# Performance work log

Hardware: AMD Instinct MI355X
Metric: run time of the kernel (lower is better)

Reference implementation:

```python
import jax, jax.numpy as jnp
import numpy as np

B, IN, OUT, STY = 8192, 2048, 2048, 512

def setup_inputs() -> dict:
    key = jax.random.key(0)
    k1, k2, k3, k4, k5 = jax.random.split(key, 5)
    bound_w = 1.0 / np.sqrt(IN)  # kaiming_uniform(a=sqrt(5)) on (OUT,IN) -> U(-1/sqrt(IN), 1/sqrt(IN))
    weight = jax.random.uniform(k1, (OUT, IN), jnp.float32, -bound_w, bound_w)
    bias = jax.random.uniform(k2, (OUT,), jnp.float32, -bound_w, bound_w)
    bound_a = 1.0 / np.sqrt(STY)
    aff_w = jax.random.uniform(k3, (2 * OUT, STY), jnp.float32, -bound_a, bound_a)
    aff_b = jnp.concatenate([jnp.ones((OUT,), jnp.float32), jnp.zeros((OUT,), jnp.float32)])
    inp = jax.random.normal(k4, (B, IN), jnp.float32)
    style = jax.random.normal(k5, (B, STY), jnp.float32)
    return {"input": inp, "style": style, "weight": weight, "bias": bias,
            "aff_w": aff_w, "aff_b": aff_b}

def reference(input, style, weight, bias, aff_w, aff_b):
    # affine: (B, 2*OUT), chunk into scale / (unused) style-bias
    enc = style @ aff_w.T + aff_b
    scale = enc[:, :OUT]  # (B, OUT); second chunk is discarded by the original forward
    # Original math: w1 = W * s[b,o]; norm = rsqrt(sum_i w1^2); w2 = w1 / norm = w1 * sqrt(sum_i w1^2)
    # sum_i (W[o,i]*s[b,o])^2 = s[b,o]^2 * rowsq[o]  ->  w2[b,o,i] = W[o,i] * s*|s| * sqrt(rowsq[o])
    rowsq = jnp.sum(weight * weight, axis=1)                  # (OUT,)
    mod = scale * jnp.abs(scale) * jnp.sqrt(rowsq)[None, :]   # (B, OUT)
    base = input @ weight.T                                   # (B, OUT) single GEMM
    return base * mod + bias[None, :]
```

## Files before the change

### kernel.cpp

```cpp
#include <hip/hip_runtime.h>
#include <cstdint>
#include <cstddef>

#define B_ROWS 8192
#define IN_DIM 2048
#define OUT_DIM 2048
#define STY_DIM 512

#define BM 128
#define BN 128
#define BK 32
#define PAD_K 40

typedef unsigned short u16;
typedef __attribute__((ext_vector_type(8))) short bf16x8;
typedef __attribute__((ext_vector_type(4))) float f32x4;

__device__ __forceinline__ void cvt_pair(float x0, float x1, uint32_t& hi, uint32_t& lo) {
  uint32_t u0 = __float_as_uint(x0), u1 = __float_as_uint(x1);
  uint32_t a0 = u0 & 0xffff0000u, a1 = u1 & 0xffff0000u;
  hi = (u0 >> 16) | a1;
  float l0 = x0 - __uint_as_float(a0);
  float l1 = x1 - __uint_as_float(a1);
  lo = (__float_as_uint(l0) >> 16) | (__float_as_uint(l1) & 0xffff0000u);
}

__device__ __forceinline__ void write_rep(const float4& v, u16* baseHi, u16* baseLo) {
  uint32_t h0, h1, l0, l1;
  cvt_pair(v.x, v.y, h0, l0);
  cvt_pair(v.z, v.w, h1, l1);
  uint2 hw; hw.x = h0; hw.y = h1;
  uint2 lw; lw.x = l0; lw.y = l1;
  *reinterpret_cast<uint2*>(baseHi) = hw;
  *reinterpret_cast<uint2*>(baseLo) = lw;
}

template<int LDK, int NT>
__device__ __forceinline__ void gemm_phase(
    const float* __restrict__ gA, const float* __restrict__ gB,
    f32x4 (&acc)[4][4],
    u16* sAhi, u16* sAlo, u16* sBhi, u16* sBlo,
    int tid)
{
  const int sr = tid >> 3;
  const int sk = (tid & 7) * 4;
  const float* pa = gA + (size_t)sr * LDK + sk;
  const float* pb = gB + (size_t)sr * LDK + sk;
  const int lbase = sr * PAD_K + sk;

  const int lane = tid & 63;
  const int wid  = tid >> 6;
  const int wr = wid >> 1, wc = wid & 1;
  const int fr = lane & 15;
  const int kg = lane >> 4;
  const int aoff = (wr * 64 + fr) * PAD_K + kg * 8;
  const int boff = (wc * 64 + fr) * PAD_K + kg * 8;

  float4 va[4], vb[4];
  #pragma unroll
  for (int rep = 0; rep < 4; ++rep) {
    va[rep] = *reinterpret_cast<const float4*>(pa + (size_t)rep * 32 * LDK);
    vb[rep] = *reinterpret_cast<const float4*>(pb + (size_t)rep * 32 * LDK);
  }
  pa += BK; pb += BK;

  for (int t = 0; t < NT; ++t) {
    __syncthreads();
    #pragma unroll
    for (int rep = 0; rep < 4; ++rep) {
      write_rep(va[rep], sAhi + lbase + rep * 32 * PAD_K, sAlo + lbase + rep * 32 * PAD_K);
      write_rep(vb[rep], sBhi + lbase + rep * 32 * PAD_K, sBlo + lbase + rep * 32 * PAD_K);
    }
    __syncthreads();
    if (t + 1 < NT) {
      #pragma unroll
      for (int rep = 0; rep < 4; ++rep) {
        va[rep] = *reinterpret_cast<const float4*>(pa + (size_t)rep * 32 * LDK);
        vb[rep] = *reinterpret_cast<const float4*>(pb + (size_t)rep * 32 * LDK);
      }
      pa += BK; pb += BK;
    }

    bf16x8 bhi[4], blo[4];
    #pragma unroll
    for (int nj = 0; nj < 4; ++nj) {
      bhi[nj] = *reinterpret_cast<const bf16x8*>(sBhi + boff + nj * 16 * PAD_K);
      blo[nj] = *reinterpret_cast<const bf16x8*>(sBlo + boff + nj * 16 * PAD_K);
    }
    #pragma unroll
    for (int mi = 0; mi < 4; ++mi) {
      bf16x8 ahi = *reinterpret_cast<const bf16x8*>(sAhi + aoff + mi * 16 * PAD_K);
      bf16x8 alo = *reinterpret_cast<const bf16x8*>(sAlo + aoff + mi * 16 * PAD_K);
      #pragma unroll
      for (int nj = 0; nj < 4; ++nj) {
        acc[mi][nj] = __builtin_amdgcn_mfma_f32_16x16x32_bf16(ahi, bhi[nj], acc[mi][nj], 0, 0, 0);
        acc[mi][nj] = __builtin_amdgcn_mfma_f32_16x16x32_bf16(ahi, blo[nj], acc[mi][nj], 0, 0, 0);
        acc[mi][nj] = __builtin_amdgcn_mfma_f32_16x16x32_bf16(alo, bhi[nj], acc[mi][nj], 0, 0, 0);
      }
    }
  }
  __syncthreads();
}

__global__ void rowsq_kernel(const float* __restrict__ w, float* __restrict__ srq) {
  int row  = blockIdx.x * 4 + (threadIdx.x >> 6);
  int lane = threadIdx.x & 63;
  const float4* p = reinterpret_cast<const float4*>(w + (size_t)row * IN_DIM);
  float s = 0.f;
  #pragma unroll
  for (int i = 0; i < 8; ++i) {
    float4 v = p[lane + i * 64];
    s += v.x * v.x + v.y * v.y + v.z * v.z + v.w * v.w;
  }
  #pragma unroll
  for (int off = 32; off > 0; off >>= 1) s += __shfl_down(s, off);
  if (lane == 0) srq[row] = sqrtf(s);
}

__global__ __launch_bounds__(256, 2) void fused_style_linear(
    const float* __restrict__ input, const float* __restrict__ style,
    const float* __restrict__ weight, const float* __restrict__ bias,
    const float* __restrict__ aff_w, const float* __restrict__ aff_b,
    const float* __restrict__ srq, float* __restrict__ out)
{
  __shared__ u16 sAhi[BM * PAD_K];
  __shared__ u16 sAlo[BM * PAD_K];
  __shared__ u16 sBhi[BN * PAD_K];
  __shared__ u16 sBlo[BN * PAD_K];

  const int tid = threadIdx.x;
  const int bn = blockIdx.x, bm = blockIdx.y;
  const int brow = bm * BM, bcol = bn * BN;

  const int lane = tid & 63, wid = tid >> 6;
  const int wr = wid >> 1, wc = wid & 1;
  const int fr = lane & 15, kg = lane >> 4;

  f32x4 sacc[4][4];
  #pragma unroll
  for (int i = 0; i < 4; ++i)
    #pragma unroll
    for (int j = 0; j < 4; ++j) {
      f32x4 z = {0.f, 0.f, 0.f, 0.f};
      sacc[i][j] = z;
    }

  gemm_phase<STY_DIM, STY_DIM / BK>(style + (size_t)brow * STY_DIM,
                                    aff_w + (size_t)bcol * STY_DIM,
                                    sacc, sAhi, sAlo, sBhi, sBlo, tid);

  float affb[4], srqv[4], biasv[4];
  #pragma unroll
  for (int nj = 0; nj < 4; ++nj) {
    int c = bcol + wc * 64 + nj * 16 + fr;
    affb[nj]  = aff_b[c];
    srqv[nj]  = srq[c];
    biasv[nj] = bias[c];
  }

  #pragma unroll
  for (int mi = 0; mi < 4; ++mi)
    #pragma unroll
    for (int nj = 0; nj < 4; ++nj)
      #pragma unroll
      for (int r = 0; r < 4; ++r) {
        float s = sacc[mi][nj][r] + affb[nj];
        sacc[mi][nj][r] = s * fabsf(s) * srqv[nj];
      }

  f32x4 acc[4][4];
  #pragma unroll
  for (int i = 0; i < 4; ++i)
    #pragma unroll
    for (int j = 0; j < 4; ++j) {
      f32x4 z = {0.f, 0.f, 0.f, 0.f};
      acc[i][j] = z;
    }

  gemm_phase<IN_DIM, IN_DIM / BK>(input + (size_t)brow * IN_DIM,
                                  weight + (size_t)bcol * IN_DIM,
                                  acc, sAhi, sAlo, sBhi, sBlo, tid);

  #pragma unroll
  for (int mi = 0; mi < 4; ++mi) {
    int r0 = brow + wr * 64 + mi * 16 + kg * 4;
    #pragma unroll
    for (int nj = 0; nj < 4; ++nj) {
      int c = bcol + wc * 64 + nj * 16 + fr;
      float* po = out + (size_t)r0 * OUT_DIM + c;
      #pragma unroll
      for (int r = 0; r < 4; ++r) {
        po[(size_t)r * OUT_DIM] = acc[mi][nj][r] * sacc[mi][nj][r] + biasv[nj];
      }
    }
  }
}

extern "C" void kernel_launch(void* const* d_in, const int* in_sizes, int n_in,
                              void* d_out, int out_size, void* d_ws, size_t ws_size,
                              hipStream_t stream) {
  (void)in_sizes; (void)n_in; (void)out_size; (void)ws_size;
  const float* input  = (const float*)d_in[0];
  const float* style  = (const float*)d_in[1];
  const float* weight = (const float*)d_in[2];
  const float* bias   = (const float*)d_in[3];
  const float* aff_w  = (const float*)d_in[4];
  const float* aff_b  = (const float*)d_in[5];
  float* out = (float*)d_out;
  float* srq = (float*)d_ws;

  rowsq_kernel<<<OUT_DIM / 4, 256, 0, stream>>>(weight, srq);

  dim3 grid(OUT_DIM / BN, B_ROWS / BM);
  fused_style_linear<<<grid, 256, 0, stream>>>(input, style, weight, bias,
                                               aff_w, aff_b, srq, out);
}
```

Baseline: 432.5 us.

## Pre-split operands to bf16 hi/lo in workspace and stream via global_load_lds

```diff
diff --git a/kernel.cpp b/kernel.cpp
--- a/kernel.cpp
+++ b/kernel.cpp
@@ -6,11 +6,6 @@
 #define IN_DIM 2048
 #define OUT_DIM 2048
 #define STY_DIM 512
-
-#define BM 128
-#define BN 128
-#define BK 32
-#define PAD_K 40
 
 typedef unsigned short u16;
 typedef __attribute__((ext_vector_type(8))) short bf16x8;
@@ -24,6 +19,180 @@
   float l1 = x1 - __uint_as_float(a1);
   lo = (__float_as_uint(l0) >> 16) | (__float_as_uint(l1) & 0xffff0000u);
 }
+
+
+__global__ void split_kernel(const float* __restrict__ src,
+                             u16* __restrict__ hi, u16* __restrict__ lo, int n4) {
+  int stride = gridDim.x * blockDim.x;
+  for (int i = blockIdx.x * blockDim.x + threadIdx.x; i < n4; i += stride) {
+    float4 v = reinterpret_cast<const float4*>(src)[i];
+    uint32_t h0, h1, l0, l1;
+    cvt_pair(v.x, v.y, h0, l0);
+    cvt_pair(v.z, v.w, h1, l1);
+    uint2 hw; hw.x = h0; hw.y = h1;
+    uint2 lw; lw.x = l0; lw.y = l1;
+    reinterpret_cast<uint2*>(hi)[i] = hw;
+    reinterpret_cast<uint2*>(lo)[i] = lw;
+  }
+}
+
+__global__ void rowsq_kernel(const float* __restrict__ w, float* __restrict__ srq) {
+  int row  = blockIdx.x * 4 + (threadIdx.x >> 6);
+  int lane = threadIdx.x & 63;
+  const float4* p = reinterpret_cast<const float4*>(w + (size_t)row * IN_DIM);
+  float s = 0.f;
+  #pragma unroll
+  for (int i = 0; i < 8; ++i) {
+    float4 v = p[lane + i * 64];
+    s += v.x * v.x + v.y * v.y + v.z * v.z + v.w * v.w;
+  }
+  #pragma unroll
+  for (int off = 32; off > 0; off >>= 1) s += __shfl_down(s, off);
+  if (lane == 0) srq[row] = sqrtf(s);
+}
+
+template<int LDK, int NT>
+__device__ __forceinline__ void gemm_bf16_phase(
+    const u16* __restrict__ gAhi, const u16* __restrict__ gAlo,
+    const u16* __restrict__ gBhi, const u16* __restrict__ gBlo,
+    f32x4 (&acc)[4][4],
+    u16* sAhi, u16* sAlo, u16* sBhi, u16* sBlo,
+    int tid)
+{
+  const int lane = tid & 63;
+  const int wid  = tid >> 6;
+  const int wr = wid >> 1, wc = wid & 1;
+  const int fr = lane & 15, kg = lane >> 4;
+
+  const u16* gsrc = (wid == 0) ? gAhi : (wid == 1) ? gAlo : (wid == 2) ? gBhi : gBlo;
+  u16* sdst = (wid == 0) ? sAhi : (wid == 1) ? sAlo : (wid == 2) ? sBhi : sBlo;
+  const u16* gl = gsrc + (size_t)(lane >> 2) * LDK + (size_t)(lane & 3) * 8;
+
+  const int aoff = (wr * 64 + fr) * 32 + kg * 8;
+  const int boff = (wc * 64 + fr) * 32 + kg * 8;
+
+  for (int t = 0; t < NT; ++t) {
+    __syncthreads();
+    {
+      const u16* g = gl + t * 32;
+      #pragma unroll
+      for (int i = 0; i < 8; ++i) {
+        __builtin_amdgcn_global_load_lds(
+            (const __attribute__((address_space(1))) void*)(g),
+            (__attribute__((address_space(3))) void*)(sdst + i * 512),
+            16, 0, 0);
+        g += (size_t)16 * LDK;
+      }
+    }
+    __syncthreads();
+
+    bf16x8 bh[4], bl[4];
+    #pragma unroll
+    for (int nj = 0; nj < 4; ++nj) {
+      bh[nj] = *reinterpret_cast<const bf16x8*>(sBhi + boff + nj * 16 * 32);
+      bl[nj] = *reinterpret_cast<const bf16x8*>(sBlo + boff + nj * 16 * 32);
+    }
+    #pragma unroll
+    for (int mi = 0; mi < 4; ++mi) {
+      bf16x8 ah = *reinterpret_cast<const bf16x8*>(sAhi + aoff + mi * 16 * 32);
+      bf16x8 al = *reinterpret_cast<const bf16x8*>(sAlo + aoff + mi * 16 * 32);
+      #pragma unroll
+      for (int nj = 0; nj < 4; ++nj) {
+        acc[mi][nj] = __builtin_amdgcn_mfma_f32_16x16x32_bf16(ah, bh[nj], acc[mi][nj], 0, 0, 0);
+        acc[mi][nj] = __builtin_amdgcn_mfma_f32_16x16x32_bf16(ah, bl[nj], acc[mi][nj], 0, 0, 0);
+        acc[mi][nj] = __builtin_amdgcn_mfma_f32_16x16x32_bf16(al, bh[nj], acc[mi][nj], 0, 0, 0);
+      }
+    }
+  }
+}
+
+__global__ __launch_bounds__(256, 2) void fused_fast(
+    const u16* __restrict__ ihi, const u16* __restrict__ ilo,
+    const u16* __restrict__ whi, const u16* __restrict__ wlo,
+    const u16* __restrict__ shi, const u16* __restrict__ slo,
+    const u16* __restrict__ awhi, const u16* __restrict__ awlo,
+    const float* __restrict__ bias, const float* __restrict__ aff_b,
+    const float* __restrict__ srq, float* __restrict__ out)
+{
+  __shared__ u16 sAhi[128 * 32];
+  __shared__ u16 sAlo[128 * 32];
+  __shared__ u16 sBhi[128 * 32];
+  __shared__ u16 sBlo[128 * 32];
+
+  const int tid = threadIdx.x;
+  const int bn = blockIdx.x, bm = blockIdx.y;
+  const int brow = bm * 128, bcol = bn * 128;
+  const int lane = tid & 63, wid = tid >> 6;
+  const int wr = wid >> 1, wc = wid & 1;
+  const int fr = lane & 15, kg = lane >> 4;
+
+  f32x4 sacc[4][4];
+  #pragma unroll
+  for (int i = 0; i < 4; ++i)
+    #pragma unroll
+    for (int j = 0; j < 4; ++j) {
+      f32x4 z = {0.f, 0.f, 0.f, 0.f};
+      sacc[i][j] = z;
+    }
+
+  gemm_bf16_phase<STY_DIM, STY_DIM / 32>(
+      shi + (size_t)brow * STY_DIM, slo + (size_t)brow * STY_DIM,
+      awhi + (size_t)bcol * STY_DIM, awlo + (size_t)bcol * STY_DIM,
+      sacc, sAhi, sAlo, sBhi, sBlo, tid);
+
+  float affb[4], srqv[4], biasv[4];
+  #pragma unroll
+  for (int nj = 0; nj < 4; ++nj) {
+    int c = bcol + wc * 64 + nj * 16 + fr;
+    affb[nj]  = aff_b[c];
+    srqv[nj]  = srq[c];
+    biasv[nj] = bias[c];
+  }
+
+  #pragma unroll
+  for (int mi = 0; mi < 4; ++mi)
+    #pragma unroll
+    for (int nj = 0; nj < 4; ++nj)
+      #pragma unroll
+      for (int r = 0; r < 4; ++r) {
+        float s = sacc[mi][nj][r] + affb[nj];
+        sacc[mi][nj][r] = s * fabsf(s) * srqv[nj];
+      }
+
+  f32x4 acc[4][4];
+  #pragma unroll
+  for (int i = 0; i < 4; ++i)
+    #pragma unroll
+    for (int j = 0; j < 4; ++j) {
+      f32x4 z = {0.f, 0.f, 0.f, 0.f};
+      acc[i][j] = z;
+    }
+
+  gemm_bf16_phase<IN_DIM, IN_DIM / 32>(
+      ihi + (size_t)brow * IN_DIM, ilo + (size_t)brow * IN_DIM,
+      whi + (size_t)bcol * IN_DIM, wlo + (size_t)bcol * IN_DIM,
+      acc, sAhi, sAlo, sBhi, sBlo, tid);
+
+  #pragma unroll
+  for (int mi = 0; mi < 4; ++mi) {
+    int r0 = brow + wr * 64 + mi * 16 + kg * 4;
+    #pragma unroll
+    for (int nj = 0; nj < 4; ++nj) {
+      int c = bcol + wc * 64 + nj * 16 + fr;
+      float* po = out + (size_t)r0 * OUT_DIM + c;
+      #pragma unroll
+      for (int r = 0; r < 4; ++r) {
+        po[(size_t)r * OUT_DIM] = acc[mi][nj][r] * sacc[mi][nj][r] + biasv[nj];
+      }
+    }
+  }
+}
+
+
+#define BMf 128
+#define BNf 128
+#define BKf 32
+#define PAD_K 40
 
 __device__ __forceinline__ void write_rep(const float4& v, u16* baseHi, u16* baseLo) {
   uint32_t h0, h1, l0, l1;
@@ -62,7 +231,7 @@
     va[rep] = *reinterpret_cast<const float4*>(pa + (size_t)rep * 32 * LDK);
     vb[rep] = *reinterpret_cast<const float4*>(pb + (size_t)rep * 32 * LDK);
   }
-  pa += BK; pb += BK;
+  pa += BKf; pb += BKf;
 
   for (int t = 0; t < NT; ++t) {
     __syncthreads();
@@ -78,7 +247,7 @@
         va[rep] = *reinterpret_cast<const float4*>(pa + (size_t)rep * 32 * LDK);
         vb[rep] = *reinterpret_cast<const float4*>(pb + (size_t)rep * 32 * LDK);
       }
-      pa += BK; pb += BK;
+      pa += BKf; pb += BKf;
     }
 
     bf16x8 bhi[4], blo[4];
@@ -100,21 +269,6 @@
     }
   }
   __syncthreads();
-}
-
-__global__ void rowsq_kernel(const float* __restrict__ w, float* __restrict__ srq) {
-  int row  = blockIdx.x * 4 + (threadIdx.x >> 6);
-  int lane = threadIdx.x & 63;
-  const float4* p = reinterpret_cast<const float4*>(w + (size_t)row * IN_DIM);
-  float s = 0.f;
-  #pragma unroll
-  for (int i = 0; i < 8; ++i) {
-    float4 v = p[lane + i * 64];
-    s += v.x * v.x + v.y * v.y + v.z * v.z + v.w * v.w;
-  }
-  #pragma unroll
-  for (int off = 32; off > 0; off >>= 1) s += __shfl_down(s, off);
-  if (lane == 0) srq[row] = sqrtf(s);
 }
 
 __global__ __launch_bounds__(256, 2) void fused_style_linear(
@@ -123,14 +277,14 @@
     const float* __restrict__ aff_w, const float* __restrict__ aff_b,
     const float* __restrict__ srq, float* __restrict__ out)
 {
-  __shared__ u16 sAhi[BM * PAD_K];
-  __shared__ u16 sAlo[BM * PAD_K];
-  __shared__ u16 sBhi[BN * PAD_K];
-  __shared__ u16 sBlo[BN * PAD_K];
+  __shared__ u16 sAhi[BMf * PAD_K];
+  __shared__ u16 sAlo[BMf * PAD_K];
+  __shared__ u16 sBhi[BNf * PAD_K];
+  __shared__ u16 sBlo[BNf * PAD_K];
 
   const int tid = threadIdx.x;
   const int bn = blockIdx.x, bm = blockIdx.y;
-  const int brow = bm * BM, bcol = bn * BN;
+  const int brow = bm * BMf, bcol = bn * BNf;
 
   const int lane = tid & 63, wid = tid >> 6;
   const int wr = wid >> 1, wc = wid & 1;
@@ -145,9 +299,9 @@
       sacc[i][j] = z;
     }
 
-  gemm_phase<STY_DIM, STY_DIM / BK>(style + (size_t)brow * STY_DIM,
-                                    aff_w + (size_t)bcol * STY_DIM,
-                                    sacc, sAhi, sAlo, sBhi, sBlo, tid);
+  gemm_phase<STY_DIM, STY_DIM / BKf>(style + (size_t)brow * STY_DIM,
+                                     aff_w + (size_t)bcol * STY_DIM,
+                                     sacc, sAhi, sAlo, sBhi, sBlo, tid);
 
   float affb[4], srqv[4], biasv[4];
   #pragma unroll
@@ -177,9 +331,9 @@
       acc[i][j] = z;
     }
 
-  gemm_phase<IN_DIM, IN_DIM / BK>(input + (size_t)brow * IN_DIM,
-                                  weight + (size_t)bcol * IN_DIM,
-                                  acc, sAhi, sAlo, sBhi, sBlo, tid);
+  gemm_phase<IN_DIM, IN_DIM / BKf>(input + (size_t)brow * IN_DIM,
+                                   weight + (size_t)bcol * IN_DIM,
+                                   acc, sAhi, sAlo, sBhi, sBlo, tid);
 
   #pragma unroll
   for (int mi = 0; mi < 4; ++mi) {
@@ -196,10 +350,11 @@
   }
 }
 
+
 extern "C" void kernel_launch(void* const* d_in, const int* in_sizes, int n_in,
                               void* d_out, int out_size, void* d_ws, size_t ws_size,
                               hipStream_t stream) {
-  (void)in_sizes; (void)n_in; (void)out_size; (void)ws_size;
+  (void)in_sizes; (void)n_in; (void)out_size;
   const float* input  = (const float*)d_in[0];
   const float* style  = (const float*)d_in[1];
   const float* weight = (const float*)d_in[2];
@@ -207,11 +362,44 @@
   const float* aff_w  = (const float*)d_in[4];
   const float* aff_b  = (const float*)d_in[5];
   float* out = (float*)d_out;
-  float* srq = (float*)d_ws;
-
-  rowsq_kernel<<<OUT_DIM / 4, 256, 0, stream>>>(weight, srq);
-
-  dim3 grid(OUT_DIM / BN, B_ROWS / BM);
-  fused_style_linear<<<grid, 256, 0, stream>>>(input, style, weight, bias,
-                                               aff_w, aff_b, srq, out);
-}
+
+  const size_t OFF_IHI = 0;
+  const size_t OFF_ILO = OFF_IHI + (size_t)B_ROWS * IN_DIM * 2;
+  const size_t OFF_WHI = OFF_ILO + (size_t)B_ROWS * IN_DIM * 2;
+  const size_t OFF_WLO = OFF_WHI + (size_t)OUT_DIM * IN_DIM * 2;
+  const size_t OFF_SHI = OFF_WLO + (size_t)OUT_DIM * IN_DIM * 2;
+  const size_t OFF_SLO = OFF_SHI + (size_t)B_ROWS * STY_DIM * 2;
+  const size_t OFF_AHI = OFF_SLO + (size_t)B_ROWS * STY_DIM * 2;
+  const size_t OFF_ALO = OFF_AHI + (size_t)OUT_DIM * STY_DIM * 2;
+  const size_t OFF_SRQ = OFF_ALO + (size_t)OUT_DIM * STY_DIM * 2;
+  const size_t WS_NEEDED = OFF_SRQ + OUT_DIM * 4;
+
+  if (ws_size >= WS_NEEDED) {
+    char* ws = (char*)d_ws;
+    u16* ihi = (u16*)(ws + OFF_IHI);
+    u16* ilo = (u16*)(ws + OFF_ILO);
+    u16* whi = (u16*)(ws + OFF_WHI);
+    u16* wlo = (u16*)(ws + OFF_WLO);
+    u16* shi = (u16*)(ws + OFF_SHI);
+    u16* slo = (u16*)(ws + OFF_SLO);
+    u16* awhi = (u16*)(ws + OFF_AHI);
+    u16* awlo = (u16*)(ws + OFF_ALO);
+    float* srq = (float*)(ws + OFF_SRQ);
+
+    split_kernel<<<2048, 256, 0, stream>>>(input,  ihi,  ilo,  B_ROWS * IN_DIM / 4);
+    split_kernel<<<2048, 256, 0, stream>>>(weight, whi,  wlo,  OUT_DIM * IN_DIM / 4);
+    split_kernel<<<2048, 256, 0, stream>>>(style,  shi,  slo,  B_ROWS * STY_DIM / 4);
+    split_kernel<<<1024, 256, 0, stream>>>(aff_w,  awhi, awlo, OUT_DIM * STY_DIM / 4);
+    rowsq_kernel<<<OUT_DIM / 4, 256, 0, stream>>>(weight, srq);
+
+    dim3 grid(OUT_DIM / 128, B_ROWS / 128);
+    fused_fast<<<grid, 256, 0, stream>>>(ihi, ilo, whi, wlo, shi, slo, awhi, awlo,
+                                         bias, aff_b, srq, out);
+  } else {
+    float* srq = (float*)d_ws;
+    rowsq_kernel<<<OUT_DIM / 4, 256, 0, stream>>>(weight, srq);
+    dim3 grid(OUT_DIM / BNf, B_ROWS / BMf);
+    fused_style_linear<<<grid, 256, 0, stream>>>(input, style, weight, bias,
+                                                 aff_w, aff_b, srq, out);
+  }
+}
```

Measured after the change: 393.7 us. -9.0%, faster.
